# Kernel optimization log

Hardware: AMD Instinct MI355X
Metric: run time of the kernel (lower is better)

## Reference

```python
import jax, jax.numpy as jnp
import numpy as np

B = 1024        # number of graphs in batch
NNODES = 64     # nodes per graph
NODE = 4        # node feature size
EDGEF = 2       # edge feature size
HID = 32        # hidden_dim
NFACT = 3       # num_factories
NE = 1024       # edges per graph (self.edges list length)


def setup_inputs() -> dict:
    key = jax.random.key(0)
    ks = jax.random.split(key, 12)
    rng = np.random.default_rng(1)
    # per-graph edge list (self.edges in the torch module)
    edges = rng.integers(0, NNODES, size=(NE, 2))
    edges_src = jnp.asarray(edges[:, 0], dtype=jnp.int32)   # [NE]
    edges_dst = jnp.asarray(edges[:, 1], dtype=jnp.int32)   # [NE]
    # batched edge_index for EdgeConv: same per-graph edges offset by b*NNODES
    offs = np.arange(B, dtype=np.int64)[:, None] * NNODES   # [B,1]
    ei_src = (edges[:, 0][None, :] + offs).reshape(-1)
    ei_dst = (edges[:, 1][None, :] + offs).reshape(-1)
    edge_index = jnp.asarray(np.stack([ei_src, ei_dst], 0), dtype=jnp.int32)  # [2, B*NE]

    N = B * NNODES
    E = B * NE
    x = jax.random.normal(ks[0], (N, NODE), dtype=jnp.float32)
    edge_attr = jax.random.normal(ks[1], (E, EDGEF), dtype=jnp.float32)
    action = jax.random.uniform(ks[2], (B, NE + NFACT), dtype=jnp.float32)

    s = 0.1
    W1 = jax.random.normal(ks[3], (2 * NODE + EDGEF, HID), dtype=jnp.float32) * s
    b1 = jnp.zeros((HID,), jnp.float32)
    W2 = jax.random.normal(ks[4], (HID, HID), dtype=jnp.float32) * s
    b2 = jnp.zeros((HID,), jnp.float32)
    D = (NODE + HID) * 2 + 1  # 73
    Wl = jax.random.normal(ks[5], (D, HID), dtype=jnp.float32) * s
    bl = jnp.zeros((HID,), jnp.float32)
    Wv = jax.random.normal(ks[6], (HID, 1), dtype=jnp.float32) * s
    bv = jnp.zeros((1,), jnp.float32)

    return {"x": x, "edge_index": edge_index, "edge_attr": edge_attr,
            "action": action, "edges_src": edges_src, "edges_dst": edges_dst,
            "W1": W1, "b1": b1, "W2": W2, "b2": b2,
            "Wl": Wl, "bl": bl, "Wv": Wv, "bv": bv}


def reference(x, edge_index, edge_attr, action, edges_src, edges_dst,
              W1, b1, W2, b2, Wl, bl, Wv, bv):
    N = x.shape[0]
    src = edge_index[0]  # flow='target_to_source': x_i = x[src], aggregate at src
    dst = edge_index[1]
    # EdgeConv message: MLP(cat[x_i, x_j, edge_attr])
    tmp = jnp.concatenate([x[src], x[dst], edge_attr], axis=1)  # [E, 10]
    msg = jax.nn.relu(tmp @ W1 + b1) @ W2 + b2                  # [E, HID]
    x_pp = jax.ops.segment_sum(msg, src, num_segments=N)        # scatter-add
    # concat node feats with conv output, split into graphs
    h = jnp.concatenate([x, x_pp], axis=1).reshape(B, NNODES, NODE + HID)  # [B,NN,36]
    # gather per-edge endpoint features
    ef = jnp.concatenate([h[:, edges_src], h[:, edges_dst]], axis=2)       # [B,NE,72]
    # factory features: last NFACT nodes duplicated
    pf = jnp.concatenate([h[:, -NFACT:], h[:, -NFACT:]], axis=-1)          # [B,NF,72]
    feats = jnp.concatenate([ef, pf], axis=1)                               # [B,NE+NF,72]
    concat = jnp.concatenate([feats, action[..., None]], axis=-1)           # [B,NE+NF,73]
    hidden = jax.nn.relu(concat @ Wl + bl)                                  # [B,NE+NF,HID]
    v = hidden @ Wv + bv                                                    # [B,NE+NF,1]
    return jnp.sum(v, axis=1).squeeze(-1)                                   # [B]
```

## Files before the change

### kernel.cpp

```cpp
#include <hip/hip_runtime.h>

#define NNODES 64
#define HID 32
#define NFACT 3
#define NE 1024
#define NROWS (NE + NFACT)
#define TPB 512
#define STR 36
#define QSTRH 20
#define MAXTILES 128
#define EPT (NE / TPB)
#define W2OFF 2560
#define WEOFF 3072
#define WPOFF 3104
#define WCOFF 4128
#define WXOFF 4160
#define WBOFF 4416

typedef short bf16x8 __attribute__((ext_vector_type(8)));
typedef float f32x4  __attribute__((ext_vector_type(4)));
typedef float f32x16 __attribute__((ext_vector_type(16)));
typedef _Float16 f16x2 __attribute__((ext_vector_type(2)));
typedef _Float16 f16x8 __attribute__((ext_vector_type(8)));

__device__ __forceinline__ unsigned pack_bf2(float lo, float hi) {
    unsigned ul = __builtin_bit_cast(unsigned, lo);
    unsigned uh = __builtin_bit_cast(unsigned, hi);
    ul += 0x7fffu + ((ul >> 16) & 1u);
    uh += 0x7fffu + ((uh >> 16) & 1u);
    return (ul >> 16) | (uh & 0xffff0000u);
}
__device__ __forceinline__ f16x2 pkrtz(float lo, float hi) {
    return __builtin_bit_cast(f16x2, __builtin_amdgcn_cvt_pkrtz(lo, hi));
}
__device__ __forceinline__ unsigned packh2u(float lo, float hi) {
    f16x2 r; r.x = (_Float16)lo; r.y = (_Float16)hi;
    return __builtin_bit_cast(unsigned, r);
}
__device__ __forceinline__ float dot2acc(f16x2 a, f16x2 b, float c) {
#if __has_builtin(__builtin_amdgcn_fdot2)
    return __builtin_amdgcn_fdot2(a, b, c, false);
#else
    return c + (float)a.x * (float)b.x + (float)a.y * (float)b.y;
#endif
}
__device__ __forceinline__ float4 fma4(float a, float4 w, float4 c) {
    c.x = fmaf(a, w.x, c.x); c.y = fmaf(a, w.y, c.y);
    c.z = fmaf(a, w.z, c.z); c.w = fmaf(a, w.w, c.w);
    return c;
}

__global__ __launch_bounds__(256) void csr_build(
    const int* __restrict__ es, const int* __restrict__ ed,
    const float* __restrict__ W1, const float* __restrict__ W2,
    const float* __restrict__ Wl, const float* __restrict__ Wv,
    const float* __restrict__ b2, int* __restrict__ gws)
{
    const int tid = threadIdx.x;
    __shared__ int sdeg[NNODES], soff[NNODES], scnt[NNODES];
    __shared__ int tns[MAXTILES], snt;
    __shared__ int pep[MAXTILES * 16];
    if (tid < NNODES) { sdeg[tid] = 0; scnt[tid] = 0; }
    if (tid < MAXTILES) tns[tid] = 0;
#pragma unroll
    for (int i = tid; i < MAXTILES * 16; i += 256) pep[i] = 0xFFF;
    int ces[4], ced[4];
#pragma unroll
    for (int i = 0; i < 4; i++) { ces[i] = es[tid + i * 256]; ced[i] = ed[tid + i * 256]; }

    unsigned* gu = (unsigned*)gws;
    float*    gf = (float*)gws;
    if (tid < 64) {
        const int s = tid >> 5, n = tid & 31;
        unsigned* o = &gu[W2OFF + tid * 8];
#pragma unroll
        for (int j = 0; j < 4; j++) {
            o[j]     = packh2u(W2[(s * 8 + 2 * j) * HID + n],      W2[(s * 8 + 2 * j + 1) * HID + n]);
            o[4 + j] = packh2u(W2[(16 + s * 8 + 2 * j) * HID + n], W2[(16 + s * 8 + 2 * j + 1) * HID + n]);
        }
    } else if (tid < 66) {
        const int s = tid - 64;
        unsigned* o = &gu[WEOFF + s * 16];
#pragma unroll
        for (int j = 0; j < 4; j++) {
            o[j]      = packh2u(W1[8 * HID + s * 8 + 2 * j],      W1[8 * HID + s * 8 + 2 * j + 1]);
            o[4 + j]  = packh2u(W1[8 * HID + 16 + s * 8 + 2 * j], W1[8 * HID + 16 + s * 8 + 2 * j + 1]);
            o[8 + j]  = packh2u(W1[9 * HID + s * 8 + 2 * j],      W1[9 * HID + s * 8 + 2 * j + 1]);
            o[12 + j] = packh2u(W1[9 * HID + 16 + s * 8 + 2 * j], W1[9 * HID + 16 + s * 8 + 2 * j + 1]);
        }
    } else if (tid < 82) {
        const int j = tid - 66;
        const float* Wl72 = Wl + 72 * HID;
        gu[WCOFF + j]      = packh2u(Wl72[j], Wl72[j + 16]);
        gu[WCOFF + 16 + j] = packh2u(Wv[j],   Wv[j + 16]);
    } else if (tid < 114) {
        gf[WBOFF + (tid - 82)] = b2[tid - 82];
    }
    if (tid < 128) {
        const int g = tid >> 6, quad = (tid >> 4) & 3, m = tid & 15;
        const int cbase = g ? 40 : 4;
        const int kh = quad * 8;
        unsigned* o = &gu[WPOFF + tid * 8];
#pragma unroll
        for (int j = 0; j < 4; j++) {
            o[j]     = pack_bf2(Wl[(cbase + kh + 2 * j) * HID + m],      Wl[(cbase + kh + 2 * j + 1) * HID + m]);
            o[4 + j] = pack_bf2(Wl[(cbase + kh + 2 * j) * HID + 16 + m], Wl[(cbase + kh + 2 * j + 1) * HID + 16 + m]);
        }
    } else if (tid < 160) {
        const int g = (tid - 128) >> 4, m = tid & 15;
        const int xbase = g ? 36 : 0;
        float* o = &gf[WXOFF + ((tid - 128)) * 8];
#pragma unroll
        for (int i = 0; i < 4; i++) {
            o[i]     = Wl[(xbase + i) * HID + m];
            o[4 + i] = Wl[(xbase + i) * HID + 16 + m];
        }
    }

    __syncthreads();
#pragma unroll
    for (int i = 0; i < 4; i++) atomicAdd(&sdeg[ces[i]], 1);
    __syncthreads();
    if (tid < NNODES) {
        const int cnt = (sdeg[tid] + 15) >> 4;
        int scan = cnt;
#pragma unroll
        for (int o = 1; o < 64; o <<= 1) {
            const int v = __shfl_up(scan, o);
            if (tid >= o) scan += v;
        }
        const int base = scan - cnt;
        soff[tid] = base;
        if (tid == NNODES - 1) snt = scan;
#pragma unroll 1
        for (int j = 0; j < cnt; j++) tns[base + j] = tid;
    }
    __syncthreads();
#pragma unroll
    for (int i = 0; i < 4; i++) {
        const int n = ces[i];
        const int idx = atomicAdd(&scnt[n], 1);
        pep[soff[n] * 16 + idx] = (tid + i * 256) | (ced[i] << 12) | (n << 18);
    }
    __syncthreads();
    if (tid < NNODES) { gws[tid] = sdeg[tid]; gws[64 + tid] = soff[tid]; }
    if (tid == 0) gws[128] = snt;
    if (tid < MAXTILES) gws[256 + tid] = tns[tid];
#pragma unroll
    for (int i = tid; i < MAXTILES * 16; i += 256) gws[512 + i] = pep[i];
}

__global__ __launch_bounds__(TPB, 6) void critic_fused(
    const float* __restrict__ x,
    const float* __restrict__ edge_attr,
    const float* __restrict__ action,
    const int*   __restrict__ es,
    const int*   __restrict__ ed,
    const float* __restrict__ W1,
    const float* __restrict__ b1,
    const float* __restrict__ bl,
    const float* __restrict__ bv,
    const int*   __restrict__ gws,
    float* __restrict__ out)
{
    const int b    = blockIdx.x;
    const int tid  = threadIdx.x;
    const int lane = tid & 63;
    const int wv   = tid >> 6;
    const int quad = lane >> 4;
    const int m16  = lane & 15;
    const f16x2 z2 = { (_Float16)0.f, (_Float16)0.f };
    const unsigned* gu = (const unsigned*)gws;
    const float*    gf = (const float*)gws;

    __shared__ __align__(16) float4 xs4[NNODES];
    __shared__ __align__(16) float  xpp[NNODES * STR];
    __shared__ __align__(16) float  qp0[NNODES * STR];
    __shared__ __align__(16) float  qp1[NNODES * STR];
    __shared__ __align__(16) float  W1s[8 * HID];
    __shared__ __align__(16) float  eas[NE * 2];
    __shared__ float  b1s[HID];
    __shared__ float  wred[TPB / 64];

    unsigned* qh0 = (unsigned*)qp0;
    unsigned* qh1 = (unsigned*)qp1;

    if (tid < NNODES) xs4[tid] = ((const float4*)x)[b * NNODES + tid];
    if (tid < 64) ((float4*)W1s)[tid] = ((const float4*)W1)[tid];
    if (tid < HID) b1s[tid] = b1[tid];
    ((float4*)eas)[tid] = ((const float4*)edge_attr)[(size_t)b * (NE / 2) + tid];
    {
        const float4 z4 = make_float4(0.f, 0.f, 0.f, 0.f);
#pragma unroll 1
        for (int i = tid; i < NNODES * STR / 4; i += TPB) ((float4*)xpp)[i] = z4;
    }

    int ces[EPT], ced[EPT];
#pragma unroll
    for (int i = 0; i < EPT; i++) {
        ces[i] = es[tid + i * TPB];
        ced[i] = ed[tid + i * TPB];
    }
    __syncthreads();

    {
        const int  n  = lane;
        const int  k0 = (wv & 3) * 8;
        const bool g1 = (wv < 4);
        const int  rb = g1 ? 0 : 4;
        const float4 xv = xs4[n];
        float4 qa, qb;
        if (g1) {
            const float4* b1v = (const float4*)&b1s[k0];
            qa = b1v[0]; qb = b1v[1];
        } else {
            qa = make_float4(0.f, 0.f, 0.f, 0.f); qb = qa;
        }
#pragma unroll 1
        for (int i = 0; i < 4; i++) {
            const float xi = (i == 0) ? xv.x : (i == 1) ? xv.y : (i == 2) ? xv.z : xv.w;
            const float4* wa = (const float4*)&W1s[(rb + i) * HID + k0];
            qa = fma4(xi, wa[0], qa); qb = fma4(xi, wa[1], qb);
        }
        uint4 p;
        p.x = __builtin_bit_cast(unsigned, pkrtz(qa.x, qa.y));
        p.y = __builtin_bit_cast(unsigned, pkrtz(qa.z, qa.w));
        p.z = __builtin_bit_cast(unsigned, pkrtz(qb.x, qb.y));
        p.w = __builtin_bit_cast(unsigned, pkrtz(qb.z, qb.w));
        unsigned* dst = g1 ? qh0 : qh1;
        *(uint4*)&dst[n * QSTRH + (wv & 3) * 4] = p;
    }
    __syncthreads();

    {
        const int* gtns = gws + 256;
        const int* gpep = gws + 512;
        const int NW   = TPB / 64;
        const int s    = lane >> 5;
        const int klo2 = s * 4;
        const int n32  = lane & 31;

        const uint4 we0 = *(const uint4*)&gu[WEOFF + s * 16];
        const uint4 we1 = *(const uint4*)&gu[WEOFF + s * 16 + 4];
        const uint4 we2 = *(const uint4*)&gu[WEOFF + s * 16 + 8];
        const uint4 we3 = *(const uint4*)&gu[WEOFF + s * 16 + 12];
        f16x2 w8p[4], w8q[4], w9p[4], w9q[4];
        w8p[0] = __builtin_bit_cast(f16x2, we0.x); w8p[1] = __builtin_bit_cast(f16x2, we0.y);
        w8p[2] = __builtin_bit_cast(f16x2, we0.z); w8p[3] = __builtin_bit_cast(f16x2, we0.w);
        w8q[0] = __builtin_bit_cast(f16x2, we1.x); w8q[1] = __builtin_bit_cast(f16x2, we1.y);
        w8q[2] = __builtin_bit_cast(f16x2, we1.z); w8q[3] = __builtin_bit_cast(f16x2, we1.w);
        w9p[0] = __builtin_bit_cast(f16x2, we2.x); w9p[1] = __builtin_bit_cast(f16x2, we2.y);
        w9p[2] = __builtin_bit_cast(f16x2, we2.z); w9p[3] = __builtin_bit_cast(f16x2, we2.w);
        w9q[0] = __builtin_bit_cast(f16x2, we3.x); w9q[1] = __builtin_bit_cast(f16x2, we3.y);
        w9q[2] = __builtin_bit_cast(f16x2, we3.z); w9q[3] = __builtin_bit_cast(f16x2, we3.w);
        const uint4 wfa = *(const uint4*)&gu[W2OFF + (s * 32 + n32) * 8];
        const uint4 wfb = *(const uint4*)&gu[W2OFF + (s * 32 + n32) * 8 + 4];
        const f16x8 hfA = __builtin_bit_cast(f16x8, wfa);
        const f16x8 hfB = __builtin_bit_cast(f16x8, wfb);

        const int np = (gws[128] + 1) >> 1;

        int p = wv;
        int raw = 0xFFF, tA = 0, tB = 0;
        if (p < np) {
            raw = gpep[p * 32 + n32];
            const int2 tt = *(const int2*)&gtns[2 * p];
            tA = tt.x; tB = tt.y;
        }
#pragma unroll 1
        while (p < np) {
            const int pn = p + NW;
            int rawn = 0xFFF, tAn = 0, tBn = 0;
            if (pn < np) {
                rawn = gpep[pn * 32 + n32];
                const int2 ttn = *(const int2*)&gtns[2 * pn];
                tAn = ttn.x; tBn = ttn.y;
            }
            const int e    = raw & 0xFFF;
            const bool pad = (e == 0xFFF);
            const int d0   = (raw >> 12) & 63;
            const int nd   = (raw >> 18) & 63;
            const float2 ea = *(const float2*)&eas[(pad ? 0 : e) * 2];

            const uint4 A1 = *(const uint4*)&qh0[nd * QSTRH + klo2];
            const uint4 A2 = *(const uint4*)&qh0[nd * QSTRH + 8 + klo2];
            const uint4 G1 = *(const uint4*)&qh1[d0 * QSTRH + klo2];
            const uint4 G2 = *(const uint4*)&qh1[d0 * QSTRH + 8 + klo2];

            const f16x2 ex2 = pkrtz(ea.x, ea.x);
            const f16x2 ey2 = pkrtz(ea.y, ea.y);
            const unsigned pz = pad ? 0u : 0xFFFFFFFFu;

            uint4 pa4, pb4;
#define MSLOT(dst, au, gu_, w8, w9) { \
            f16x2 t = __builtin_bit_cast(f16x2, au) + __builtin_bit_cast(f16x2, gu_); \
            t = __builtin_elementwise_fma(ex2, w8, t); \
            t = __builtin_elementwise_fma(ey2, w9, t); \
            t = __builtin_elementwise_max(t, z2); \
            dst = __builtin_bit_cast(unsigned, t) & pz; }
            MSLOT(pa4.x, A1.x, G1.x, w8p[0], w9p[0])
            MSLOT(pa4.y, A1.y, G1.y, w8p[1], w9p[1])
            MSLOT(pa4.z, A1.z, G1.z, w8p[2], w9p[2])
            MSLOT(pa4.w, A1.w, G1.w, w8p[3], w9p[3])
            MSLOT(pb4.x, A2.x, G2.x, w8q[0], w9q[0])
            MSLOT(pb4.y, A2.y, G2.y, w8q[1], w9q[1])
            MSLOT(pb4.z, A2.z, G2.z, w8q[2], w9q[2])
            MSLOT(pb4.w, A2.w, G2.w, w8q[3], w9q[3])
#undef MSLOT
            const f16x8 afA = __builtin_bit_cast(f16x8, pa4);
            const f16x8 afB = __builtin_bit_cast(f16x8, pb4);

            f32x16 c;
#pragma unroll
            for (int j = 0; j < 16; j++) c[j] = 0.0f;
            c = __builtin_amdgcn_mfma_f32_32x32x16_f16(afA, hfA, c, 0, 0, 0);
            c = __builtin_amdgcn_mfma_f32_32x32x16_f16(afB, hfB, c, 0, 0, 0);

            float sA = ((c[0] + c[1]) + (c[2] + c[3])) + ((c[4] + c[5]) + (c[6] + c[7]));
            float sB = ((c[8] + c[9]) + (c[10] + c[11])) + ((c[12] + c[13]) + (c[14] + c[15]));
            sA += __shfl_xor(sA, 32);
            sB += __shfl_xor(sB, 32);
            const int   nst = (lane < 32) ? tA : tB;
            const float sv  = (lane < 32) ? sA : sB;
            atomicAdd(&xpp[nst * STR + n32], sv);

            p = pn; raw = rawn; tA = tAn; tB = tBn;
        }
    }
    __syncthreads();

    const bool g1p = (wv < 4);
    const int  g   = g1p ? 0 : 1;
    const int  pidx = ((g * 4 + quad) * 16 + m16) * 8;
    const uint4 bpau = *(const uint4*)&gu[WPOFF + pidx];
    const uint4 bpbu = *(const uint4*)&gu[WPOFF + pidx + 4];
    const bf16x8 bPa = __builtin_bit_cast(bf16x8, bpau);
    const bf16x8 bPb = __builtin_bit_cast(bf16x8, bpbu);
    const float4 wxav = *(const float4*)&gf[WXOFF + (g * 16 + m16) * 8];
    const float4 wxbv = *(const float4*)&gf[WXOFF + (g * 16 + m16) * 8 + 4];
    const float4 b2a = *(const float4*)&gf[WBOFF + quad * 8];
    const float4 b2b = *(const float4*)&gf[WBOFF + quad * 8 + 4];
    const float bca = g1p ? bl[m16] : 0.f;
    const float bcb = g1p ? bl[16 + m16] : 0.f;
    const int   mrow = (wv & 3) * 16 + m16;
    const float dn   = (float)gws[mrow];

    {
        const int kh = quad * 8;
        const float4* xr = (const float4*)&xpp[mrow * STR + kh];
        float4 x0 = xr[0], x1 = xr[1];
        x0.x = fmaf(dn, b2a.x, x0.x); x0.y = fmaf(dn, b2a.y, x0.y);
        x0.z = fmaf(dn, b2a.z, x0.z); x0.w = fmaf(dn, b2a.w, x0.w);
        x1.x = fmaf(dn, b2b.x, x1.x); x1.y = fmaf(dn, b2b.y, x1.y);
        x1.z = fmaf(dn, b2b.z, x1.z); x1.w = fmaf(dn, b2b.w, x1.w);
        uint4 packed;
        packed.x = pack_bf2(x0.x, x0.y);
        packed.y = pack_bf2(x0.z, x0.w);
        packed.z = pack_bf2(x1.x, x1.y);
        packed.w = pack_bf2(x1.z, x1.w);
        const bf16x8 af = __builtin_bit_cast(bf16x8, packed);

        float wxa[4] = { wxav.x, wxav.y, wxav.z, wxav.w };
        float wxb[4] = { wxbv.x, wxbv.y, wxbv.z, wxbv.w };
        f32x4 ca, cb;
#pragma unroll
        for (int r = 0; r < 4; r++) {
            const float4 xv = xs4[(wv & 3) * 16 + quad * 4 + r];
            float a0 = bca, a1 = bcb;
#pragma unroll
            for (int i = 0; i < 4; i++) {
                const float xi = (i == 0) ? xv.x : (i == 1) ? xv.y : (i == 2) ? xv.z : xv.w;
                a0 = fmaf(xi, wxa[i], a0);
                a1 = fmaf(xi, wxb[i], a1);
            }
            ca[r] = a0; cb[r] = a1;
        }
        ca = __builtin_amdgcn_mfma_f32_16x16x32_bf16(af, bPa, ca, 0, 0, 0);
        cb = __builtin_amdgcn_mfma_f32_16x16x32_bf16(af, bPb, cb, 0, 0, 0);

        __syncthreads();
        unsigned* dsth = g1p ? qh0 : qh1;
#pragma unroll
        for (int r = 0; r < 4; r++) {
            const int row = (wv & 3) * 16 + quad * 4 + r;
            dsth[row * QSTRH + m16] = __builtin_bit_cast(unsigned, pkrtz(ca[r], cb[r]));
        }
    }
    __syncthreads();

    float vsum = 0.0f;
    {
        const float* actb = action + (size_t)b * NROWS;
        const float bvv = bv[0];
        f16x2 wlh[16], wvh[16];
#pragma unroll
        for (int q = 0; q < 4; q++) {
            const uint4 ul = *(const uint4*)&gu[WCOFF + q * 4];
            const uint4 uv = *(const uint4*)&gu[WCOFF + 16 + q * 4];
            wlh[q*4+0] = __builtin_bit_cast(f16x2, ul.x); wlh[q*4+1] = __builtin_bit_cast(f16x2, ul.y);
            wlh[q*4+2] = __builtin_bit_cast(f16x2, ul.z); wlh[q*4+3] = __builtin_bit_cast(f16x2, ul.w);
            wvh[q*4+0] = __builtin_bit_cast(f16x2, uv.x); wvh[q*4+1] = __builtin_bit_cast(f16x2, uv.y);
            wvh[q*4+2] = __builtin_bit_cast(f16x2, uv.z); wvh[q*4+3] = __builtin_bit_cast(f16x2, uv.w);
        }

#define CSLOT(j, pu, qu, acc) { \
        f16x2 t = __builtin_bit_cast(f16x2, pu) + __builtin_bit_cast(f16x2, qu); \
        t = __builtin_elementwise_fma(a2, wlh[j], t); \
        t = __builtin_elementwise_max(t, z2); \
        acc = dot2acc(t, wvh[j], acc); }

#define CROW(na, nb, av) { \
        const unsigned* ra = &qh0[(na) * QSTRH]; \
        const unsigned* rb = &qh1[(nb) * QSTRH]; \
        const uint4 Pa0 = *(const uint4*)&ra[0]; \
        const uint4 Pa1 = *(const uint4*)&ra[4]; \
        const uint4 Pa2 = *(const uint4*)&ra[8]; \
        const uint4 Pa3 = *(const uint4*)&ra[12]; \
        const uint4 Pb0 = *(const uint4*)&rb[0]; \
        const uint4 Pb1 = *(const uint4*)&rb[4]; \
        const uint4 Pb2 = *(const uint4*)&rb[8]; \
        const uint4 Pb3 = *(const uint4*)&rb[12]; \
        const f16x2 a2 = pkrtz(av, av); \
        float v0 = bvv, v1 = 0.0f; \
        CSLOT( 0, Pa0.x, Pb0.x, v0) CSLOT( 1, Pa0.y, Pb0.y, v1) \
        CSLOT( 2, Pa0.z, Pb0.z, v0) CSLOT( 3, Pa0.w, Pb0.w, v1) \
        CSLOT( 4, Pa1.x, Pb1.x, v0) CSLOT( 5, Pa1.y, Pb1.y, v1) \
        CSLOT( 6, Pa1.z, Pb1.z, v0) CSLOT( 7, Pa1.w, Pb1.w, v1) \
        CSLOT( 8, Pa2.x, Pb2.x, v0) CSLOT( 9, Pa2.y, Pb2.y, v1) \
        CSLOT(10, Pa2.z, Pb2.z, v0) CSLOT(11, Pa2.w, Pb2.w, v1) \
        CSLOT(12, Pa3.x, Pb3.x, v0) CSLOT(13, Pa3.y, Pb3.y, v1) \
        CSLOT(14, Pa3.z, Pb3.z, v0) CSLOT(15, Pa3.w, Pb3.w, v1) \
        vsum += v0 + v1; }

#pragma unroll 1
        for (int i = 0; i < EPT; i++) {
            const int na = ces[i], nb = ced[i];
            const float a = actb[tid + i * TPB];
            CROW(na, nb, a)
        }
        if (tid < NFACT) {
            const int r = NE + tid;
            const int naf = NNODES - NFACT + tid;
            const float av = actb[r];
            CROW(naf, naf, av)
        }
#undef CROW
#undef CSLOT
    }

#pragma unroll
    for (int off = 32; off > 0; off >>= 1)
        vsum += __shfl_down(vsum, off, 64);
    if ((tid & 63) == 0) wred[tid >> 6] = vsum;
    __syncthreads();
    if (tid == 0) {
        float t = 0.0f;
#pragma unroll
        for (int w = 0; w < TPB / 64; w++) t += wred[w];
        out[b] = t;
    }
}

extern "C" void kernel_launch(void* const* d_in, const int* in_sizes, int n_in,
                              void* d_out, int out_size, void* d_ws, size_t ws_size,
                              hipStream_t stream) {
    const float* x         = (const float*)d_in[0];
    const float* edge_attr = (const float*)d_in[2];
    const float* action    = (const float*)d_in[3];
    const int*   es        = (const int*)d_in[4];
    const int*   ed        = (const int*)d_in[5];
    const float* W1        = (const float*)d_in[6];
    const float* b1        = (const float*)d_in[7];
    const float* W2        = (const float*)d_in[8];
    const float* b2        = (const float*)d_in[9];
    const float* Wl        = (const float*)d_in[10];
    const float* bl        = (const float*)d_in[11];
    const float* Wv        = (const float*)d_in[12];
    const float* bv        = (const float*)d_in[13];
    float* out = (float*)d_out;
    int*   gws = (int*)d_ws;

    csr_build<<<dim3(1), dim3(256), 0, stream>>>(es, ed, W1, W2, Wl, Wv, b2, gws);
    critic_fused<<<dim3(out_size), dim3(TPB), 0, stream>>>(
        x, edge_attr, action, es, ed, W1, b1, bl, bv, gws, out);
}
```

Before: 123.9 us.

## Split fused critic kernel into graph-conv and value kernels via global buffer

```diff
diff --git a/kernel.cpp b/kernel.cpp
--- a/kernel.cpp
+++ b/kernel.cpp
@@ -9,13 +9,13 @@
 #define STR 36
 #define QSTRH 20
 #define MAXTILES 128
-#define EPT (NE / TPB)
 #define W2OFF 2560
 #define WEOFF 3072
 #define WPOFF 3104
 #define WCOFF 4128
 #define WXOFF 4160
 #define WBOFF 4416
+#define GWSN  4448
 
 typedef short bf16x8 __attribute__((ext_vector_type(8)));
 typedef float f32x4  __attribute__((ext_vector_type(4)));
@@ -150,18 +150,14 @@
     for (int i = tid; i < MAXTILES * 16; i += 256) gws[512 + i] = pep[i];
 }
 
-__global__ __launch_bounds__(TPB, 6) void critic_fused(
+__global__ __launch_bounds__(TPB, 6) void critic_graph(
     const float* __restrict__ x,
     const float* __restrict__ edge_attr,
-    const float* __restrict__ action,
-    const int*   __restrict__ es,
-    const int*   __restrict__ ed,
     const float* __restrict__ W1,
     const float* __restrict__ b1,
     const float* __restrict__ bl,
-    const float* __restrict__ bv,
     const int*   __restrict__ gws,
-    float* __restrict__ out)
+    unsigned*    __restrict__ gP)
 {
     const int b    = blockIdx.x;
     const int tid  = threadIdx.x;
@@ -180,7 +176,6 @@
     __shared__ __align__(16) float  W1s[8 * HID];
     __shared__ __align__(16) float  eas[NE * 2];
     __shared__ float  b1s[HID];
-    __shared__ float  wred[TPB / 64];
 
     unsigned* qh0 = (unsigned*)qp0;
     unsigned* qh1 = (unsigned*)qp1;
@@ -193,13 +188,6 @@
         const float4 z4 = make_float4(0.f, 0.f, 0.f, 0.f);
 #pragma unroll 1
         for (int i = tid; i < NNODES * STR / 4; i += TPB) ((float4*)xpp)[i] = z4;
-    }
-
-    int ces[EPT], ced[EPT];
-#pragma unroll
-    for (int i = 0; i < EPT; i++) {
-        ces[i] = es[tid + i * TPB];
-        ced[i] = ed[tid + i * TPB];
     }
     __syncthreads();
 
@@ -329,23 +317,23 @@
     }
     __syncthreads();
 
-    const bool g1p = (wv < 4);
-    const int  g   = g1p ? 0 : 1;
-    const int  pidx = ((g * 4 + quad) * 16 + m16) * 8;
-    const uint4 bpau = *(const uint4*)&gu[WPOFF + pidx];
-    const uint4 bpbu = *(const uint4*)&gu[WPOFF + pidx + 4];
-    const bf16x8 bPa = __builtin_bit_cast(bf16x8, bpau);
-    const bf16x8 bPb = __builtin_bit_cast(bf16x8, bpbu);
-    const float4 wxav = *(const float4*)&gf[WXOFF + (g * 16 + m16) * 8];
-    const float4 wxbv = *(const float4*)&gf[WXOFF + (g * 16 + m16) * 8 + 4];
-    const float4 b2a = *(const float4*)&gf[WBOFF + quad * 8];
-    const float4 b2b = *(const float4*)&gf[WBOFF + quad * 8 + 4];
-    const float bca = g1p ? bl[m16] : 0.f;
-    const float bcb = g1p ? bl[16 + m16] : 0.f;
-    const int   mrow = (wv & 3) * 16 + m16;
-    const float dn   = (float)gws[mrow];
-
     {
+        const bool g1p = (wv < 4);
+        const int  g   = g1p ? 0 : 1;
+        const int  pidx = ((g * 4 + quad) * 16 + m16) * 8;
+        const uint4 bpau = *(const uint4*)&gu[WPOFF + pidx];
+        const uint4 bpbu = *(const uint4*)&gu[WPOFF + pidx + 4];
+        const bf16x8 bPa = __builtin_bit_cast(bf16x8, bpau);
+        const bf16x8 bPb = __builtin_bit_cast(bf16x8, bpbu);
+        const float4 wxav = *(const float4*)&gf[WXOFF + (g * 16 + m16) * 8];
+        const float4 wxbv = *(const float4*)&gf[WXOFF + (g * 16 + m16) * 8 + 4];
+        const float4 b2a = *(const float4*)&gf[WBOFF + quad * 8];
+        const float4 b2b = *(const float4*)&gf[WBOFF + quad * 8 + 4];
+        const float bca = g1p ? bl[m16] : 0.f;
+        const float bcb = g1p ? bl[16 + m16] : 0.f;
+        const int   mrow = (wv & 3) * 16 + m16;
+        const float dn   = (float)gws[mrow];
+
         const int kh = quad * 8;
         const float4* xr = (const float4*)&xpp[mrow * STR + kh];
         float4 x0 = xr[0], x1 = xr[1];
@@ -378,75 +366,92 @@
         ca = __builtin_amdgcn_mfma_f32_16x16x32_bf16(af, bPa, ca, 0, 0, 0);
         cb = __builtin_amdgcn_mfma_f32_16x16x32_bf16(af, bPb, cb, 0, 0, 0);
 
-        __syncthreads();
-        unsigned* dsth = g1p ? qh0 : qh1;
+        unsigned* grow = gP + ((size_t)b * 2 + g) * (NNODES * 16);
 #pragma unroll
         for (int r = 0; r < 4; r++) {
             const int row = (wv & 3) * 16 + quad * 4 + r;
-            dsth[row * QSTRH + m16] = __builtin_bit_cast(unsigned, pkrtz(ca[r], cb[r]));
-        }
-    }
-    __syncthreads();
+            grow[row * 16 + m16] = __builtin_bit_cast(unsigned, pkrtz(ca[r], cb[r]));
+        }
+    }
+}
+
+__global__ __launch_bounds__(TPB, 6) void critic_value(
+    const float* __restrict__ action,
+    const int*   __restrict__ es,
+    const int*   __restrict__ ed,
+    const float* __restrict__ bv,
+    const int*   __restrict__ gws,
+    const unsigned* __restrict__ gP,
+    float* __restrict__ out)
+{
+    const int b   = blockIdx.x;
+    const int tid = threadIdx.x;
+    const f16x2 z2 = { (_Float16)0.f, (_Float16)0.f };
+    const unsigned* gu = (const unsigned*)gws;
+    __shared__ float wred[TPB / 64];
+
+    const float* actb = action + (size_t)b * NROWS;
+    const float bvv = bv[0];
+    const unsigned* P1 = gP + (size_t)b * 2 * (NNODES * 16);
+    const unsigned* P2 = P1 + NNODES * 16;
+
+    f16x2 wlh[16], wvh[16];
+#pragma unroll
+    for (int q = 0; q < 4; q++) {
+        const uint4 ul = *(const uint4*)&gu[WCOFF + q * 4];
+        const uint4 uv = *(const uint4*)&gu[WCOFF + 16 + q * 4];
+        wlh[q*4+0] = __builtin_bit_cast(f16x2, ul.x); wlh[q*4+1] = __builtin_bit_cast(f16x2, ul.y);
+        wlh[q*4+2] = __builtin_bit_cast(f16x2, ul.z); wlh[q*4+3] = __builtin_bit_cast(f16x2, ul.w);
+        wvh[q*4+0] = __builtin_bit_cast(f16x2, uv.x); wvh[q*4+1] = __builtin_bit_cast(f16x2, uv.y);
+        wvh[q*4+2] = __builtin_bit_cast(f16x2, uv.z); wvh[q*4+3] = __builtin_bit_cast(f16x2, uv.w);
+    }
 
     float vsum = 0.0f;
-    {
-        const float* actb = action + (size_t)b * NROWS;
-        const float bvv = bv[0];
-        f16x2 wlh[16], wvh[16];
-#pragma unroll
-        for (int q = 0; q < 4; q++) {
-            const uint4 ul = *(const uint4*)&gu[WCOFF + q * 4];
-            const uint4 uv = *(const uint4*)&gu[WCOFF + 16 + q * 4];
-            wlh[q*4+0] = __builtin_bit_cast(f16x2, ul.x); wlh[q*4+1] = __builtin_bit_cast(f16x2, ul.y);
-            wlh[q*4+2] = __builtin_bit_cast(f16x2, ul.z); wlh[q*4+3] = __builtin_bit_cast(f16x2, ul.w);
-            wvh[q*4+0] = __builtin_bit_cast(f16x2, uv.x); wvh[q*4+1] = __builtin_bit_cast(f16x2, uv.y);
-            wvh[q*4+2] = __builtin_bit_cast(f16x2, uv.z); wvh[q*4+3] = __builtin_bit_cast(f16x2, uv.w);
-        }
 
 #define CSLOT(j, pu, qu, acc) { \
-        f16x2 t = __builtin_bit_cast(f16x2, pu) + __builtin_bit_cast(f16x2, qu); \
-        t = __builtin_elementwise_fma(a2, wlh[j], t); \
-        t = __builtin_elementwise_max(t, z2); \
-        acc = dot2acc(t, wvh[j], acc); }
+    f16x2 t = __builtin_bit_cast(f16x2, pu) + __builtin_bit_cast(f16x2, qu); \
+    t = __builtin_elementwise_fma(a2, wlh[j], t); \
+    t = __builtin_elementwise_max(t, z2); \
+    acc = dot2acc(t, wvh[j], acc); }
 
 #define CROW(na, nb, av) { \
-        const unsigned* ra = &qh0[(na) * QSTRH]; \
-        const unsigned* rb = &qh1[(nb) * QSTRH]; \
-        const uint4 Pa0 = *(const uint4*)&ra[0]; \
-        const uint4 Pa1 = *(const uint4*)&ra[4]; \
-        const uint4 Pa2 = *(const uint4*)&ra[8]; \
-        const uint4 Pa3 = *(const uint4*)&ra[12]; \
-        const uint4 Pb0 = *(const uint4*)&rb[0]; \
-        const uint4 Pb1 = *(const uint4*)&rb[4]; \
-        const uint4 Pb2 = *(const uint4*)&rb[8]; \
-        const uint4 Pb3 = *(const uint4*)&rb[12]; \
-        const f16x2 a2 = pkrtz(av, av); \
-        float v0 = bvv, v1 = 0.0f; \
-        CSLOT( 0, Pa0.x, Pb0.x, v0) CSLOT( 1, Pa0.y, Pb0.y, v1) \
-        CSLOT( 2, Pa0.z, Pb0.z, v0) CSLOT( 3, Pa0.w, Pb0.w, v1) \
-        CSLOT( 4, Pa1.x, Pb1.x, v0) CSLOT( 5, Pa1.y, Pb1.y, v1) \
-        CSLOT( 6, Pa1.z, Pb1.z, v0) CSLOT( 7, Pa1.w, Pb1.w, v1) \
-        CSLOT( 8, Pa2.x, Pb2.x, v0) CSLOT( 9, Pa2.y, Pb2.y, v1) \
-        CSLOT(10, Pa2.z, Pb2.z, v0) CSLOT(11, Pa2.w, Pb2.w, v1) \
-        CSLOT(12, Pa3.x, Pb3.x, v0) CSLOT(13, Pa3.y, Pb3.y, v1) \
-        CSLOT(14, Pa3.z, Pb3.z, v0) CSLOT(15, Pa3.w, Pb3.w, v1) \
-        vsum += v0 + v1; }
+    const unsigned* ra = &P1[(na) * 16]; \
+    const unsigned* rb = &P2[(nb) * 16]; \
+    const uint4 Pa0 = *(const uint4*)&ra[0]; \
+    const uint4 Pa1 = *(const uint4*)&ra[4]; \
+    const uint4 Pa2 = *(const uint4*)&ra[8]; \
+    const uint4 Pa3 = *(const uint4*)&ra[12]; \
+    const uint4 Pb0 = *(const uint4*)&rb[0]; \
+    const uint4 Pb1 = *(const uint4*)&rb[4]; \
+    const uint4 Pb2 = *(const uint4*)&rb[8]; \
+    const uint4 Pb3 = *(const uint4*)&rb[12]; \
+    const f16x2 a2 = pkrtz(av, av); \
+    float v0 = bvv, v1 = 0.0f; \
+    CSLOT( 0, Pa0.x, Pb0.x, v0) CSLOT( 1, Pa0.y, Pb0.y, v1) \
+    CSLOT( 2, Pa0.z, Pb0.z, v0) CSLOT( 3, Pa0.w, Pb0.w, v1) \
+    CSLOT( 4, Pa1.x, Pb1.x, v0) CSLOT( 5, Pa1.y, Pb1.y, v1) \
+    CSLOT( 6, Pa1.z, Pb1.z, v0) CSLOT( 7, Pa1.w, Pb1.w, v1) \
+    CSLOT( 8, Pa2.x, Pb2.x, v0) CSLOT( 9, Pa2.y, Pb2.y, v1) \
+    CSLOT(10, Pa2.z, Pb2.z, v0) CSLOT(11, Pa2.w, Pb2.w, v1) \
+    CSLOT(12, Pa3.x, Pb3.x, v0) CSLOT(13, Pa3.y, Pb3.y, v1) \
+    CSLOT(14, Pa3.z, Pb3.z, v0) CSLOT(15, Pa3.w, Pb3.w, v1) \
+    vsum += v0 + v1; }
 
 #pragma unroll 1
-        for (int i = 0; i < EPT; i++) {
-            const int na = ces[i], nb = ced[i];
-            const float a = actb[tid + i * TPB];
-            CROW(na, nb, a)
-        }
-        if (tid < NFACT) {
-            const int r = NE + tid;
-            const int naf = NNODES - NFACT + tid;
-            const float av = actb[r];
-            CROW(naf, naf, av)
-        }
+    for (int i = 0; i < NE / TPB; i++) {
+        const int r = tid + i * TPB;
+        const int na = es[r], nb = ed[r];
+        const float a = actb[r];
+        CROW(na, nb, a)
+    }
+    if (tid < NFACT) {
+        const int r = NE + tid;
+        const int naf = NNODES - NFACT + tid;
+        const float av = actb[r];
+        CROW(naf, naf, av)
+    }
 #undef CROW
 #undef CSLOT
-    }
 
 #pragma unroll
     for (int off = 32; off > 0; off >>= 1)
@@ -478,9 +483,12 @@
     const float* Wv        = (const float*)d_in[12];
     const float* bv        = (const float*)d_in[13];
     float* out = (float*)d_out;
-    int*   gws = (int*)d_ws;
+    int*      gws = (int*)d_ws;
+    unsigned* gP  = (unsigned*)((int*)d_ws + GWSN);
 
     csr_build<<<dim3(1), dim3(256), 0, stream>>>(es, ed, W1, W2, Wl, Wv, b2, gws);
-    critic_fused<<<dim3(out_size), dim3(TPB), 0, stream>>>(
-        x, edge_attr, action, es, ed, W1, b1, bl, bv, gws, out);
-}
+    critic_graph<<<dim3(out_size), dim3(TPB), 0, stream>>>(
+        x, edge_attr, W1, b1, bl, gws, gP);
+    critic_value<<<dim3(out_size), dim3(TPB), 0, stream>>>(
+        action, es, ed, bv, gws, gP, out);
+}
```

Measured after the change: 132.8 us. 1.07x slower.
